# Kernel optimization log

Measured on AMD Instinct MI355X. Metric: run time of the kernel, lower is better.

Reference implementation:

```python
import jax, jax.numpy as jnp
import numpy as np
from jax import lax

FIR_TAPS = np.array([1.0, 3.0, 3.0, 1.0], dtype=np.float32)
FACTOR = 2
GAIN = 1.0


def _fir_kernel(C):
    # _setup_kernel: outer product, normalize to sum 1; upsample scales by gain*factor**2
    k = np.outer(FIR_TAPS, FIR_TAPS)
    k = k / k.sum() * (GAIN * FACTOR ** 2)  # 4x4 kernel, sum == 4
    k = jnp.asarray(k, jnp.float32)
    return jnp.tile(k[None, None], (C, 1, 1, 1))  # [C,1,4,4] depthwise


def setup_inputs() -> dict:
    key = jax.random.key(0)
    k1, k2, k3 = jax.random.split(key, 3)
    x = jax.random.normal(k1, (16, 256, 64, 64), jnp.float32)
    W = jax.random.normal(k2, (256, 256, 3, 3), jnp.float32) * 0.02
    b = jax.random.normal(k3, (256,), jnp.float32) * 0.02
    return {"x": x, "W": W, "b": b}


def reference(x, W, b):
    B, C, H, Wd = x.shape
    kern = _fir_kernel(C)
    # upfirdn2d upsample: zero-insert by 2 (lhs_dilation), pad0=2 / pad1=1(+up-1=2),
    # depthwise FIR correlation -> [B, C, 2H, 2W]
    p0, p1 = 2, 2  # pad1 = p//2 + (factor-1) trailing zeros folded into padding
    h = lax.conv_general_dilated(
        x, kern, window_strides=(1, 1), padding=((p0, p1), (p0, p1)),
        lhs_dilation=(FACTOR, FACTOR),
        dimension_numbers=("NCHW", "OIHW", "NCHW"), feature_group_count=C)
    # 3x3 conv, padding=1, stride=1 -> [B, out_ch, 2H, 2W]
    y = lax.conv_general_dilated(
        h, W, window_strides=(1, 1), padding=((1, 1), (1, 1)),
        dimension_numbers=("NCHW", "OIHW", "NCHW"))
    return y + b[None, :, None, None]
```

## Files before the change

### kernel.cpp

```cpp
#include <hip/hip_runtime.h>
#include <hip/hip_bf16.h>
#include <stdint.h>

typedef __attribute__((ext_vector_type(8))) short bf16x8;
typedef __attribute__((ext_vector_type(4))) float f32x4;

#define PH 130
#define NT 36
#define ITERS 18

__device__ __forceinline__ short f2bf(float f) {
  uint32_t u = __builtin_bit_cast(uint32_t, f);
  u = (u + 0x7FFFu + ((u >> 16) & 1u)) >> 16;
  return (short)u;
}

__device__ __forceinline__ uint32_t pack2bf(float lo, float hi) {
  return ((uint32_t)(uint16_t)f2bf(hi) << 16) | (uint16_t)f2bf(lo);
}

__device__ __forceinline__ void gload16(const void* g, void* l) {
  __builtin_amdgcn_global_load_lds(
      (const __attribute__((address_space(1))) void*)g,
      (__attribute__((address_space(3))) void*)l, 16, 0, 0);
}

__global__ void wpack(const float* __restrict__ W, short* __restrict__ A) {
  int tid = blockIdx.x * 256 + threadIdx.x;
  if (tid >= 256 * 2304) return;
  int co = tid / 2304;
  int r  = tid - co * 2304;
  int tap = r >> 8, ci = r & 255;
  A[tid] = f2bf(W[((size_t)(co * 256 + ci)) * 9 + tap]);
}

__global__ void fir_up(const float* __restrict__ x, short* __restrict__ hT) {
  const int bp = blockIdx.x;
  const int b = bp / PH, pp = bp - b * PH;
  const int ci0 = blockIdx.y << 6;
  const int t = threadIdx.x;
  short* outrow = hT + ((size_t)(b * PH + pp) * PH) * 256 + ci0;

  if (pp == 0 || pp == PH - 1) {
    for (int idx = t; idx < PH * 32; idx += 256) {
      int qp = idx >> 5, c2 = idx & 31;
      *(uint32_t*)&outrow[(size_t)qp * 256 + c2 * 2] = 0u;
    }
    return;
  }
  const int p = pp - 1;
  int i0, i1; float wr0, wr1;
  if (!(p & 1)) { i0 = (p >> 1) - 1; i1 = p >> 1;     wr0 = 0.25f; wr1 = 0.75f; }
  else          { i0 = p >> 1;       i1 = (p >> 1)+1; wr0 = 0.75f; wr1 = 0.25f; }

  __shared__ float X[2][64][65];
#pragma unroll
  for (int r = 0; r < 2; ++r) {
    int ir = r ? i1 : i0;
    bool ok = (ir >= 0 && ir < 64);
#pragma unroll
    for (int it = 0; it < 4; ++it) {
      int idx = it * 256 + t;
      int ci = idx >> 4, jq = idx & 15;
      f32x4 v = {0.f, 0.f, 0.f, 0.f};
      if (ok)
        v = *(const f32x4*)&x[((size_t)(b * 256 + ci0 + ci) * 64 + ir) * 64 + jq * 4];
      X[r][jq * 4 + 0][ci] = v[0];
      X[r][jq * 4 + 1][ci] = v[1];
      X[r][jq * 4 + 2][ci] = v[2];
      X[r][jq * 4 + 3][ci] = v[3];
    }
  }
  __syncthreads();

  {
    float* base = &X[0][0][0];
#pragma unroll
    for (int it = 0; it < 16; ++it) {
      int idx = it * 256 + t;
      int a = idx + (idx >> 6);
      base[a] = wr0 * base[a] + wr1 * base[a + 64 * 65];
    }
  }
  __syncthreads();

  const int c2 = (t & 31) * 2;
  const int qg = t >> 5;
  for (int qp = qg; qp < PH; qp += 8) {
    uint32_t out = 0u;
    if (qp >= 1 && qp <= 128) {
      int q = qp - 1;
      int par = q & 1;
      int jb = (q >> 1) - 1 + par;
      float wc0 = par ? 0.75f : 0.25f;
      float wc1 = par ? 0.25f : 0.75f;
      float v00 = 0.f, v01 = 0.f, v10 = 0.f, v11 = 0.f;
      if (jb >= 0)     { v00 = X[0][jb][c2];     v01 = X[0][jb][c2 + 1]; }
      if (jb + 1 < 64) { v10 = X[0][jb + 1][c2]; v11 = X[0][jb + 1][c2 + 1]; }
      out = pack2bf(wc0 * v00 + wc1 * v10, wc0 * v01 + wc1 * v11);
    }
    *(uint32_t*)&outrow[(size_t)qp * 256 + c2] = out;
  }
}

__global__ __launch_bounds__(512) void conv3x3_gemm(
    const short* __restrict__ hT, const short* __restrict__ Wp,
    const float* __restrict__ bias, float* __restrict__ y) {
  __shared__ short ldsA[2][16384];
  __shared__ short ldsB[2][16384];
  const int tid = threadIdx.x;
  const int lane = tid & 63, w = tid >> 6;
  const int wm = w >> 2, wn = w & 3;

  const int bid = blockIdx.x;
  const int tau = (bid & 7) * 128 + (bid >> 3);
  const int b = tau >> 6, p0 = (tau & 63) * 2;

  const short* srcA[4];
  const short* srcB[4];
#pragma unroll
  for (int h = 0; h < 2; ++h)
#pragma unroll
    for (int i = 0; i < 2; ++i) {
      int o = h * 16384 + i * 8192 + w * 1024 + lane * 16;
      int L = o ^ (((o >> 7) & 7) << 4);
      int row = L >> 7, kk = (L & 127) >> 1;
      srcA[h * 2 + i] = hT + ((size_t)((b * PH + p0 + (row >> 7)) * PH + (row & 127))) * 256 + kk;
      srcB[h * 2 + i] = Wp + (size_t)row * 2304 + kk;
    }

  auto offA = [&](int t) {
    int tap = t >> 2, ci0 = (t & 3) << 6;
    int dm = (tap >= 6) ? 2 : (tap >= 3) ? 1 : 0;
    int dn = tap - 3 * dm;
    return (dm * PH + dn) * 256 + ci0;
  };
  auto offB = [&](int t) { return (t >> 2) * 256 + ((t & 3) << 6); };

  auto stageA = [&](int t, int h) {
    int o = offA(t);
    short* dst = &ldsA[t & 1][h * 8192];
#pragma unroll
    for (int i = 0; i < 2; ++i)
      gload16(srcA[h * 2 + i] + o, dst + i * 4096 + w * 512);
  };
  auto stageB = [&](int t, int h) {
    int o = offB(t);
    short* dst = &ldsB[t & 1][h * 8192];
#pragma unroll
    for (int i = 0; i < 2; ++i)
      gload16(srcB[h * 2 + i] + o, dst + i * 4096 + w * 512);
  };

  int aP[2], bP[2];
#pragma unroll
  for (int ks = 0; ks < 2; ++ks) {
    int La = (wm * 128 + (lane & 15)) * 128 + (lane >> 4) * 16 + ks * 64;
    aP[ks] = La ^ ((lane & 7) << 4);
    int Lb = (wn * 64 + (lane & 15)) * 128 + (lane >> 4) * 16 + ks * 64;
    bP[ks] = Lb ^ ((lane & 7) << 4);
  }

  const char* LA0 = (const char*)&ldsA[0][0];
  const char* LB0 = (const char*)&ldsB[0][0];
  const char* LA1 = (const char*)&ldsA[1][0];
  const char* LB1 = (const char*)&ldsB[1][0];

  stageA(0, 0); stageB(0, 0); stageB(0, 1); stageA(0, 1);
  stageA(1, 0); stageB(1, 0); stageB(1, 1);
  asm volatile("s_waitcnt vmcnt(6)" ::: "memory");
  __builtin_amdgcn_s_barrier();

  f32x4 acc[8][4];
#pragma unroll
  for (int m = 0; m < 8; ++m)
#pragma unroll
    for (int n = 0; n < 4; ++n) acc[m][n] = (f32x4){0.f, 0.f, 0.f, 0.f};

  for (int i = 0; i < ITERS; ++i) {
    const int u = 2 * i, v = u + 1;
    const bool more = (u + 2 < NT);
    bf16x8 a_[2][4], c_[2][4], b_[2][2], b2[2][2];

#pragma unroll
    for (int ks = 0; ks < 2; ++ks) {
#pragma unroll
      for (int m = 0; m < 4; ++m) a_[ks][m] = *(const bf16x8*)(LA0 + aP[ks] + m * 2048);
#pragma unroll
      for (int n = 0; n < 2; ++n) b_[ks][n] = *(const bf16x8*)(LB0 + bP[ks] + n * 2048);
    }
    stageA(v, 1);
    __builtin_amdgcn_s_barrier();
    asm volatile("s_waitcnt lgkmcnt(0)" ::: "memory");
    __builtin_amdgcn_s_setprio(1);
#pragma unroll
    for (int m = 0; m < 4; ++m)
#pragma unroll
      for (int n = 0; n < 2; ++n) {
        acc[m][n] = __builtin_amdgcn_mfma_f32_16x16x32_bf16(a_[0][m], b_[0][n], acc[m][n], 0, 0, 0);
        acc[m][n] = __builtin_amdgcn_mfma_f32_16x16x32_bf16(a_[1][m], b_[1][n], acc[m][n], 0, 0, 0);
      }
    __builtin_amdgcn_s_setprio(0);
    __builtin_amdgcn_s_barrier();

#pragma unroll
    for (int ks = 0; ks < 2; ++ks)
#pragma unroll
      for (int n = 0; n < 2; ++n) b2[ks][n] = *(const bf16x8*)(LB0 + bP[ks] + (n + 2) * 2048);
    __builtin_amdgcn_s_barrier();
    asm volatile("s_waitcnt lgkmcnt(0)" ::: "memory");
    __builtin_amdgcn_s_setprio(1);
#pragma unroll
    for (int m = 0; m < 4; ++m)
#pragma unroll
      for (int n = 0; n < 2; ++n) {
        acc[m][n + 2] = __builtin_amdgcn_mfma_f32_16x16x32_bf16(a_[0][m], b2[0][n], acc[m][n + 2], 0, 0, 0);
        acc[m][n + 2] = __builtin_amdgcn_mfma_f32_16x16x32_bf16(a_[1][m], b2[1][n], acc[m][n + 2], 0, 0, 0);
      }
    __builtin_amdgcn_s_setprio(0);
    __builtin_amdgcn_s_barrier();

#pragma unroll
    for (int ks = 0; ks < 2; ++ks)
#pragma unroll
      for (int m = 0; m < 4; ++m) c_[ks][m] = *(const bf16x8*)(LA0 + aP[ks] + (m + 4) * 2048);
    if (more) stageB(u + 2, 0);
    __builtin_amdgcn_s_barrier();
    asm volatile("s_waitcnt lgkmcnt(0)" ::: "memory");
    __builtin_amdgcn_s_setprio(1);
#pragma unroll
    for (int m = 0; m < 4; ++m)
#pragma unroll
      for (int n = 0; n < 2; ++n) {
        acc[m + 4][n] = __builtin_amdgcn_mfma_f32_16x16x32_bf16(c_[0][m], b_[0][n], acc[m + 4][n], 0, 0, 0);
        acc[m + 4][n] = __builtin_amdgcn_mfma_f32_16x16x32_bf16(c_[1][m], b_[1][n], acc[m + 4][n], 0, 0, 0);
      }
    __builtin_amdgcn_s_setprio(0);
    __builtin_amdgcn_s_barrier();

    if (more) { stageB(u + 2, 1); stageA(u + 2, 0); }
    __builtin_amdgcn_s_barrier();
    __builtin_amdgcn_s_setprio(1);
#pragma unroll
    for (int m = 0; m < 4; ++m)
#pragma unroll
      for (int n = 0; n < 2; ++n) {
        acc[m + 4][n + 2] = __builtin_amdgcn_mfma_f32_16x16x32_bf16(c_[0][m], b2[0][n], acc[m + 4][n + 2], 0, 0, 0);
        acc[m + 4][n + 2] = __builtin_amdgcn_mfma_f32_16x16x32_bf16(c_[1][m], b2[1][n], acc[m + 4][n + 2], 0, 0, 0);
      }
    __builtin_amdgcn_s_setprio(0);
    if (more) asm volatile("s_waitcnt vmcnt(6)" ::: "memory");
    else      asm volatile("s_waitcnt vmcnt(0)" ::: "memory");
    __builtin_amdgcn_s_barrier();

#pragma unroll
    for (int ks = 0; ks < 2; ++ks) {
#pragma unroll
      for (int m = 0; m < 4; ++m) a_[ks][m] = *(const bf16x8*)(LA1 + aP[ks] + m * 2048);
#pragma unroll
      for (int n = 0; n < 2; ++n) b_[ks][n] = *(const bf16x8*)(LB1 + bP[ks] + n * 2048);
    }
    if (more) stageA(u + 2, 1);
    __builtin_amdgcn_s_barrier();
    asm volatile("s_waitcnt lgkmcnt(0)" ::: "memory");
    __builtin_amdgcn_s_setprio(1);
#pragma unroll
    for (int m = 0; m < 4; ++m)
#pragma unroll
      for (int n = 0; n < 2; ++n) {
        acc[m][n] = __builtin_amdgcn_mfma_f32_16x16x32_bf16(a_[0][m], b_[0][n], acc[m][n], 0, 0, 0);
        acc[m][n] = __builtin_amdgcn_mfma_f32_16x16x32_bf16(a_[1][m], b_[1][n], acc[m][n], 0, 0, 0);
      }
    __builtin_amdgcn_s_setprio(0);
    __builtin_amdgcn_s_barrier();

#pragma unroll
    for (int ks = 0; ks < 2; ++ks)
#pragma unroll
      for (int n = 0; n < 2; ++n) b2[ks][n] = *(const bf16x8*)(LB1 + bP[ks] + (n + 2) * 2048);
    __builtin_amdgcn_s_barrier();
    asm volatile("s_waitcnt lgkmcnt(0)" ::: "memory");
    __builtin_amdgcn_s_setprio(1);
#pragma unroll
    for (int m = 0; m < 4; ++m)
#pragma unroll
      for (int n = 0; n < 2; ++n) {
        acc[m][n + 2] = __builtin_amdgcn_mfma_f32_16x16x32_bf16(a_[0][m], b2[0][n], acc[m][n + 2], 0, 0, 0);
        acc[m][n + 2] = __builtin_amdgcn_mfma_f32_16x16x32_bf16(a_[1][m], b2[1][n], acc[m][n + 2], 0, 0, 0);
      }
    __builtin_amdgcn_s_setprio(0);
    __builtin_amdgcn_s_barrier();

#pragma unroll
    for (int ks = 0; ks < 2; ++ks)
#pragma unroll
      for (int m = 0; m < 4; ++m) c_[ks][m] = *(const bf16x8*)(LA1 + aP[ks] + (m + 4) * 2048);
    if (more) stageB(u + 3, 0);
    __builtin_amdgcn_s_barrier();
    asm volatile("s_waitcnt lgkmcnt(0)" ::: "memory");
    __builtin_amdgcn_s_setprio(1);
#pragma unroll
    for (int m = 0; m < 4; ++m)
#pragma unroll
      for (int n = 0; n < 2; ++n) {
        acc[m + 4][n] = __builtin_amdgcn_mfma_f32_16x16x32_bf16(c_[0][m], b_[0][n], acc[m + 4][n], 0, 0, 0);
        acc[m + 4][n] = __builtin_amdgcn_mfma_f32_16x16x32_bf16(c_[1][m], b_[1][n], acc[m + 4][n], 0, 0, 0);
      }
    __builtin_amdgcn_s_setprio(0);
    __builtin_amdgcn_s_barrier();

    if (more) { stageB(u + 3, 1); stageA(u + 3, 0); }
    __builtin_amdgcn_s_barrier();
    __builtin_amdgcn_s_setprio(1);
#pragma unroll
    for (int m = 0; m < 4; ++m)
#pragma unroll
      for (int n = 0; n < 2; ++n) {
        acc[m + 4][n + 2] = __builtin_amdgcn_mfma_f32_16x16x32_bf16(c_[0][m], b2[0][n], acc[m + 4][n + 2], 0, 0, 0);
        acc[m + 4][n + 2] = __builtin_amdgcn_mfma_f32_16x16x32_bf16(c_[1][m], b2[1][n], acc[m + 4][n + 2], 0, 0, 0);
      }
    __builtin_amdgcn_s_setprio(0);
    if (more) asm volatile("s_waitcnt vmcnt(6)" ::: "memory");
    __builtin_amdgcn_s_barrier();
  }

#pragma unroll
  for (int n = 0; n < 4; ++n) {
    int co = wn * 64 + n * 16 + (lane & 15);
    float bv = bias[co];
    float* yp = y + (((size_t)(b * 256 + co)) * 128 + (p0 + wm)) * 128;
#pragma unroll
    for (int m = 0; m < 8; ++m) {
      int q0 = m * 16 + ((lane >> 4) << 2);
      f32x4 vv = acc[m][n];
      vv[0] += bv; vv[1] += bv; vv[2] += bv; vv[3] += bv;
      *(f32x4*)(yp + q0) = vv;
    }
  }
}

extern "C" void kernel_launch(void* const* d_in, const int* in_sizes, int n_in,
                              void* d_out, int out_size, void* d_ws, size_t ws_size,
                              hipStream_t stream) {
  const float* x    = (const float*)d_in[0];
  const float* W    = (const float*)d_in[1];
  const float* bias = (const float*)d_in[2];
  float* y = (float*)d_out;

  const size_t hT_bytes = (size_t)16 * PH * PH * 256 * 2;
  const size_t A_bytes  = (size_t)256 * 2304 * 2;
  if (ws_size < hT_bytes + A_bytes) return;

  short* hT = (short*)d_ws;
  short* Wp = (short*)((char*)d_ws + hT_bytes);

  wpack<<<(256 * 2304 + 255) / 256, 256, 0, stream>>>(W, Wp);
  dim3 g1(16 * PH, 4);
  fir_up<<<g1, 256, 0, stream>>>(x, hT);
  conv3x3_gemm<<<1024, 512, 0, stream>>>(hT, Wp, bias, y);
}
```

Before: 390.6 us.

## Switch GEMM main loop to 32x32x16 MFMA with fewer pipeline phases

Replaces the 16x16x32 bf16 MFMA tiling with 32x32x16 MFMA (f32x16 accumulators). LDS read addressing and the epilogue store mapping change to match. The per-stage schedule drops from four compute phases to two per buffer, with fewer barriers, and A/B staging is merged into whole-tile loads with adjusted vmcnt waits. The aim is to cut LDS reads per FLOP and barrier/sync overhead, at the risk of lower issue overlap and different LDS bank-conflict behaviour.

```diff
diff --git a/kernel.cpp b/kernel.cpp
--- a/kernel.cpp
+++ b/kernel.cpp
@@ -4,6 +4,7 @@
 
 typedef __attribute__((ext_vector_type(8))) short bf16x8;
 typedef __attribute__((ext_vector_type(4))) float f32x4;
+typedef __attribute__((ext_vector_type(16))) float f32x16;
 
 #define PH 130
 #define NT 36
@@ -137,28 +138,28 @@
   };
   auto offB = [&](int t) { return (t >> 2) * 256 + ((t & 3) << 6); };
 
-  auto stageA = [&](int t, int h) {
+  auto stageA = [&](int t) {
     int o = offA(t);
-    short* dst = &ldsA[t & 1][h * 8192];
-#pragma unroll
-    for (int i = 0; i < 2; ++i)
-      gload16(srcA[h * 2 + i] + o, dst + i * 4096 + w * 512);
+    short* dst = &ldsA[t & 1][0];
+#pragma unroll
+    for (int j = 0; j < 4; ++j)
+      gload16(srcA[j] + o, dst + (j >> 1) * 8192 + (j & 1) * 4096 + w * 512);
   };
-  auto stageB = [&](int t, int h) {
+  auto stageB = [&](int t) {
     int o = offB(t);
-    short* dst = &ldsB[t & 1][h * 8192];
-#pragma unroll
-    for (int i = 0; i < 2; ++i)
-      gload16(srcB[h * 2 + i] + o, dst + i * 4096 + w * 512);
+    short* dst = &ldsB[t & 1][0];
+#pragma unroll
+    for (int j = 0; j < 4; ++j)
+      gload16(srcB[j] + o, dst + (j >> 1) * 8192 + (j & 1) * 4096 + w * 512);
   };
 
-  int aP[2], bP[2];
-#pragma unroll
-  for (int ks = 0; ks < 2; ++ks) {
-    int La = (wm * 128 + (lane & 15)) * 128 + (lane >> 4) * 16 + ks * 64;
-    aP[ks] = La ^ ((lane & 7) << 4);
-    int Lb = (wn * 64 + (lane & 15)) * 128 + (lane >> 4) * 16 + ks * 64;
-    bP[ks] = Lb ^ ((lane & 7) << 4);
+  int aPk[4], bPk[4];
+#pragma unroll
+  for (int ks = 0; ks < 4; ++ks) {
+    int La = (wm * 128 + (lane & 31)) * 128 + (lane >> 5) * 16 + ks * 32;
+    aPk[ks] = La ^ (((La >> 7) & 7) << 4);
+    int Lb = (wn * 64 + (lane & 31)) * 128 + (lane >> 5) * 16 + ks * 32;
+    bPk[ks] = Lb ^ (((Lb >> 7) & 7) << 4);
   }
 
   const char* LA0 = (const char*)&ldsA[0][0];
@@ -166,175 +167,130 @@
   const char* LA1 = (const char*)&ldsA[1][0];
   const char* LB1 = (const char*)&ldsB[1][0];
 
-  stageA(0, 0); stageB(0, 0); stageB(0, 1); stageA(0, 1);
-  stageA(1, 0); stageB(1, 0); stageB(1, 1);
-  asm volatile("s_waitcnt vmcnt(6)" ::: "memory");
+  f32x16 acc[4][2];
+#pragma unroll
+  for (int m = 0; m < 4; ++m)
+#pragma unroll
+    for (int n = 0; n < 2; ++n) acc[m][n] = (f32x16)(0.f);
+
+  stageB(0); stageA(0); stageB(1);
+  asm volatile("s_waitcnt vmcnt(4)" ::: "memory");
   __builtin_amdgcn_s_barrier();
 
-  f32x4 acc[8][4];
-#pragma unroll
-  for (int m = 0; m < 8; ++m)
-#pragma unroll
-    for (int n = 0; n < 4; ++n) acc[m][n] = (f32x4){0.f, 0.f, 0.f, 0.f};
-
   for (int i = 0; i < ITERS; ++i) {
-    const int u = 2 * i, v = u + 1;
-    const bool more = (u + 2 < NT);
-    bf16x8 a_[2][4], c_[2][4], b_[2][2], b2[2][2];
-
-#pragma unroll
-    for (int ks = 0; ks < 2; ++ks) {
-#pragma unroll
-      for (int m = 0; m < 4; ++m) a_[ks][m] = *(const bf16x8*)(LA0 + aP[ks] + m * 2048);
-#pragma unroll
-      for (int n = 0; n < 2; ++n) b_[ks][n] = *(const bf16x8*)(LB0 + bP[ks] + n * 2048);
-    }
-    stageA(v, 1);
+    const int u = 2 * i;
+    const bool more2 = (u + 2 < NT), more3 = (u + 3 < NT);
+    bf16x8 a_[2][4], b_[2][4];
+
+#pragma unroll
+    for (int m = 0; m < 2; ++m)
+#pragma unroll
+      for (int ks = 0; ks < 4; ++ks)
+        a_[m][ks] = *(const bf16x8*)(LA0 + aPk[ks] + m * 4096);
+#pragma unroll
+    for (int n = 0; n < 2; ++n)
+#pragma unroll
+      for (int ks = 0; ks < 4; ++ks)
+        b_[n][ks] = *(const bf16x8*)(LB0 + bPk[ks] + n * 4096);
+    stageA(u + 1);
     __builtin_amdgcn_s_barrier();
     asm volatile("s_waitcnt lgkmcnt(0)" ::: "memory");
     __builtin_amdgcn_s_setprio(1);
 #pragma unroll
-    for (int m = 0; m < 4; ++m)
-#pragma unroll
-      for (int n = 0; n < 2; ++n) {
-        acc[m][n] = __builtin_amdgcn_mfma_f32_16x16x32_bf16(a_[0][m], b_[0][n], acc[m][n], 0, 0, 0);
-        acc[m][n] = __builtin_amdgcn_mfma_f32_16x16x32_bf16(a_[1][m], b_[1][n], acc[m][n], 0, 0, 0);
-      }
+    for (int m = 0; m < 2; ++m)
+#pragma unroll
+      for (int n = 0; n < 2; ++n)
+#pragma unroll
+        for (int ks = 0; ks < 4; ++ks)
+          acc[m][n] = __builtin_amdgcn_mfma_f32_32x32x16_bf16(a_[m][ks], b_[n][ks], acc[m][n], 0, 0, 0);
     __builtin_amdgcn_s_setprio(0);
     __builtin_amdgcn_s_barrier();
 
-#pragma unroll
-    for (int ks = 0; ks < 2; ++ks)
-#pragma unroll
-      for (int n = 0; n < 2; ++n) b2[ks][n] = *(const bf16x8*)(LB0 + bP[ks] + (n + 2) * 2048);
+    bf16x8 c_[2][4];
+#pragma unroll
+    for (int m = 0; m < 2; ++m)
+#pragma unroll
+      for (int ks = 0; ks < 4; ++ks)
+        c_[m][ks] = *(const bf16x8*)(LA0 + aPk[ks] + (m + 2) * 4096);
+    if (more2) stageB(u + 2);
     __builtin_amdgcn_s_barrier();
     asm volatile("s_waitcnt lgkmcnt(0)" ::: "memory");
     __builtin_amdgcn_s_setprio(1);
 #pragma unroll
-    for (int m = 0; m < 4; ++m)
-#pragma unroll
-      for (int n = 0; n < 2; ++n) {
-        acc[m][n + 2] = __builtin_amdgcn_mfma_f32_16x16x32_bf16(a_[0][m], b2[0][n], acc[m][n + 2], 0, 0, 0);
-        acc[m][n + 2] = __builtin_amdgcn_mfma_f32_16x16x32_bf16(a_[1][m], b2[1][n], acc[m][n + 2], 0, 0, 0);
-      }
+    for (int m = 0; m < 2; ++m)
+#pragma unroll
+      for (int n = 0; n < 2; ++n)
+#pragma unroll
+        for (int ks = 0; ks < 4; ++ks)
+          acc[m + 2][n] = __builtin_amdgcn_mfma_f32_32x32x16_bf16(c_[m][ks], b_[n][ks], acc[m + 2][n], 0, 0, 0);
     __builtin_amdgcn_s_setprio(0);
-    __builtin_amdgcn_s_barrier();
-
-#pragma unroll
-    for (int ks = 0; ks < 2; ++ks)
-#pragma unroll
-      for (int m = 0; m < 4; ++m) c_[ks][m] = *(const bf16x8*)(LA0 + aP[ks] + (m + 4) * 2048);
-    if (more) stageB(u + 2, 0);
+    if (more2) asm volatile("s_waitcnt vmcnt(4)" ::: "memory");
+    else       asm volatile("s_waitcnt vmcnt(0)" ::: "memory");
+    __builtin_amdgcn_s_barrier();
+
+#pragma unroll
+    for (int m = 0; m < 2; ++m)
+#pragma unroll
+      for (int ks = 0; ks < 4; ++ks)
+        a_[m][ks] = *(const bf16x8*)(LA1 + aPk[ks] + m * 4096);
+#pragma unroll
+    for (int n = 0; n < 2; ++n)
+#pragma unroll
+      for (int ks = 0; ks < 4; ++ks)
+        b_[n][ks] = *(const bf16x8*)(LB1 + bPk[ks] + n * 4096);
+    if (more2) stageA(u + 2);
     __builtin_amdgcn_s_barrier();
     asm volatile("s_waitcnt lgkmcnt(0)" ::: "memory");
     __builtin_amdgcn_s_setprio(1);
 #pragma unroll
-    for (int m = 0; m < 4; ++m)
-#pragma unroll
-      for (int n = 0; n < 2; ++n) {
-        acc[m + 4][n] = __builtin_amdgcn_mfma_f32_16x16x32_bf16(c_[0][m], b_[0][n], acc[m + 4][n], 0, 0, 0);
-        acc[m + 4][n] = __builtin_amdgcn_mfma_f32_16x16x32_bf16(c_[1][m], b_[1][n], acc[m + 4][n], 0, 0, 0);
-      }
+    for (int m = 0; m < 2; ++m)
+#pragma unroll
+      for (int n = 0; n < 2; ++n)
+#pragma unroll
+        for (int ks = 0; ks < 4; ++ks)
+          acc[m][n] = __builtin_amdgcn_mfma_f32_32x32x16_bf16(a_[m][ks], b_[n][ks], acc[m][n], 0, 0, 0);
     __builtin_amdgcn_s_setprio(0);
     __builtin_amdgcn_s_barrier();
 
-    if (more) { stageB(u + 2, 1); stageA(u + 2, 0); }
-    __builtin_amdgcn_s_barrier();
-    __builtin_amdgcn_s_setprio(1);
-#pragma unroll
-    for (int m = 0; m < 4; ++m)
-#pragma unroll
-      for (int n = 0; n < 2; ++n) {
-        acc[m + 4][n + 2] = __builtin_amdgcn_mfma_f32_16x16x32_bf16(c_[0][m], b2[0][n], acc[m + 4][n + 2], 0, 0, 0);
-        acc[m + 4][n + 2] = __builtin_amdgcn_mfma_f32_16x16x32_bf16(c_[1][m], b2[1][n], acc[m + 4][n + 2], 0, 0, 0);
-      }
-    __builtin_amdgcn_s_setprio(0);
-    if (more) asm volatile("s_waitcnt vmcnt(6)" ::: "memory");
-    else      asm volatile("s_waitcnt vmcnt(0)" ::: "memory");
-    __builtin_amdgcn_s_barrier();
-
-#pragma unroll
-    for (int ks = 0; ks < 2; ++ks) {
-#pragma unroll
-      for (int m = 0; m < 4; ++m) a_[ks][m] = *(const bf16x8*)(LA1 + aP[ks] + m * 2048);
-#pragma unroll
-      for (int n = 0; n < 2; ++n) b_[ks][n] = *(const bf16x8*)(LB1 + bP[ks] + n * 2048);
-    }
-    if (more) stageA(u + 2, 1);
+#pragma unroll
+    for (int m = 0; m < 2; ++m)
+#pragma unroll
+      for (int ks = 0; ks < 4; ++ks)
+        c_[m][ks] = *(const bf16x8*)(LA1 + aPk[ks] + (m + 2) * 4096);
+    if (more3) stageB(u + 3);
     __builtin_amdgcn_s_barrier();
     asm volatile("s_waitcnt lgkmcnt(0)" ::: "memory");
     __builtin_amdgcn_s_setprio(1);
 #pragma unroll
-    for (int m = 0; m < 4; ++m)
-#pragma unroll
-      for (int n = 0; n < 2; ++n) {
-        acc[m][n] = __builtin_amdgcn_mfma_f32_16x16x32_bf16(a_[0][m], b_[0][n], acc[m][n], 0, 0, 0);
-        acc[m][n] = __builtin_amdgcn_mfma_f32_16x16x32_bf16(a_[1][m], b_[1][n], acc[m][n], 0, 0, 0);
-      }
+    for (int m = 0; m < 2; ++m)
+#pragma unroll
+      for (int n = 0; n < 2; ++n)
+#pragma unroll
+        for (int ks = 0; ks < 4; ++ks)
+          acc[m + 2][n] = __builtin_amdgcn_mfma_f32_32x32x16_bf16(c_[m][ks], b_[n][ks], acc[m + 2][n], 0, 0, 0);
     __builtin_amdgcn_s_setprio(0);
-    __builtin_amdgcn_s_barrier();
-
-#pragma unroll
-    for (int ks = 0; ks < 2; ++ks)
-#pragma unroll
-      for (int n = 0; n < 2; ++n) b2[ks][n] = *(const bf16x8*)(LB1 + bP[ks] + (n + 2) * 2048);
-    __builtin_amdgcn_s_barrier();
-    asm volatile("s_waitcnt lgkmcnt(0)" ::: "memory");
-    __builtin_amdgcn_s_setprio(1);
-#pragma unroll
-    for (int m = 0; m < 4; ++m)
-#pragma unroll
-      for (int n = 0; n < 2; ++n) {
-        acc[m][n + 2] = __builtin_amdgcn_mfma_f32_16x16x32_bf16(a_[0][m], b2[0][n], acc[m][n + 2], 0, 0, 0);
-        acc[m][n + 2] = __builtin_amdgcn_mfma_f32_16x16x32_bf16(a_[1][m], b2[1][n], acc[m][n + 2], 0, 0, 0);
-      }
-    __builtin_amdgcn_s_setprio(0);
-    __builtin_amdgcn_s_barrier();
-
-#pragma unroll
-    for (int ks = 0; ks < 2; ++ks)
-#pragma unroll
-      for (int m = 0; m < 4; ++m) c_[ks][m] = *(const bf16x8*)(LA1 + aP[ks] + (m + 4) * 2048);
-    if (more) stageB(u + 3, 0);
-    __builtin_amdgcn_s_barrier();
-    asm volatile("s_waitcnt lgkmcnt(0)" ::: "memory");
-    __builtin_amdgcn_s_setprio(1);
-#pragma unroll
-    for (int m = 0; m < 4; ++m)
-#pragma unroll
-      for (int n = 0; n < 2; ++n) {
-        acc[m + 4][n] = __builtin_amdgcn_mfma_f32_16x16x32_bf16(c_[0][m], b_[0][n], acc[m + 4][n], 0, 0, 0);
-        acc[m + 4][n] = __builtin_amdgcn_mfma_f32_16x16x32_bf16(c_[1][m], b_[1][n], acc[m + 4][n], 0, 0, 0);
-      }
-    __builtin_amdgcn_s_setprio(0);
-    __builtin_amdgcn_s_barrier();
-
-    if (more) { stageB(u + 3, 1); stageA(u + 3, 0); }
-    __builtin_amdgcn_s_barrier();
-    __builtin_amdgcn_s_setprio(1);
-#pragma unroll
-    for (int m = 0; m < 4; ++m)
-#pragma unroll
-      for (int n = 0; n < 2; ++n) {
-        acc[m + 4][n + 2] = __builtin_amdgcn_mfma_f32_16x16x32_bf16(c_[0][m], b2[0][n], acc[m + 4][n + 2], 0, 0, 0);
-        acc[m + 4][n + 2] = __builtin_amdgcn_mfma_f32_16x16x32_bf16(c_[1][m], b2[1][n], acc[m + 4][n + 2], 0, 0, 0);
-      }
-    __builtin_amdgcn_s_setprio(0);
-    if (more) asm volatile("s_waitcnt vmcnt(6)" ::: "memory");
-    __builtin_amdgcn_s_barrier();
-  }
-
-#pragma unroll
-  for (int n = 0; n < 4; ++n) {
-    int co = wn * 64 + n * 16 + (lane & 15);
+    if (more3) asm volatile("s_waitcnt vmcnt(4)" ::: "memory");
+    else       asm volatile("s_waitcnt vmcnt(0)" ::: "memory");
+    __builtin_amdgcn_s_barrier();
+  }
+
+#pragma unroll
+  for (int n = 0; n < 2; ++n) {
+    int co = wn * 64 + n * 32 + (lane & 31);
     float bv = bias[co];
     float* yp = y + (((size_t)(b * 256 + co)) * 128 + (p0 + wm)) * 128;
 #pragma unroll
-    for (int m = 0; m < 8; ++m) {
-      int q0 = m * 16 + ((lane >> 4) << 2);
-      f32x4 vv = acc[m][n];
-      vv[0] += bv; vv[1] += bv; vv[2] += bv; vv[3] += bv;
-      *(f32x4*)(yp + q0) = vv;
+    for (int m = 0; m < 4; ++m) {
+#pragma unroll
+      for (int rq = 0; rq < 4; ++rq) {
+        int q0 = m * 32 + rq * 8 + ((lane >> 5) << 2);
+        f32x4 vv;
+        vv[0] = acc[m][n][rq * 4 + 0] + bv;
+        vv[1] = acc[m][n][rq * 4 + 1] + bv;
+        vv[2] = acc[m][n][rq * 4 + 2] + bv;
+        vv[3] = acc[m][n][rq * 4 + 3] + bv;
+        *(f32x4*)(yp + q0) = vv;
+      }
     }
   }
 }
```

Result: slower. 433.5 us (+11.0%).
